# Performance work log

Hardware: AMD Instinct MI355X
Metric: run time of the kernel (lower is better)

The kernel has to match this reference:

```python
import jax, jax.numpy as jnp
import numpy as np

NF, DG, K = 32, 8, 9  # channels, deformable groups, kernel taps (3x3)


def conv2d(x, w, b, stride=1):
    out = jax.lax.conv_general_dilated(x, w, (stride, stride), ((1, 1), (1, 1)),
                                       dimension_numbers=('NCHW', 'OIHW', 'NCHW'))
    return out + b[None, :, None, None]


def lrelu(x):
    return jnp.where(x >= 0, x, 0.1 * x)


def dcn(x, off_fea, om_w, om_b, w, b):
    """Modulated deformable conv v2 (DCN_sep): offsets/mask predicted from off_fea."""
    B, C, H, W = x.shape
    om = conv2d(off_fea, om_w, om_b).reshape(B, DG, 3, K, H, W)
    off_y, off_x = om[:, :, 0], om[:, :, 1]          # [B,DG,K,H,W]
    mask = jax.nn.sigmoid(om[:, :, 2])               # [B,DG,K,H,W]
    ky = (jnp.arange(K) // 3 - 1).astype(x.dtype)    # kernel tap dy in {-1,0,1}
    kx = (jnp.arange(K) % 3 - 1).astype(x.dtype)
    py = off_y + jnp.arange(H, dtype=x.dtype)[:, None] + ky[:, None, None]
    px = off_x + jnp.arange(W, dtype=x.dtype) + kx[:, None, None]
    y0 = jnp.floor(py); x0 = jnp.floor(px)
    dy = py - y0; dx = px - x0
    Cg = C // DG
    xg = x.reshape(B, DG, Cg, H * W)

    def gather(yi, xi):
        valid = ((yi >= 0) & (yi <= H - 1) & (xi >= 0) & (xi <= W - 1)).astype(x.dtype)
        idx = (jnp.clip(yi, 0, H - 1).astype(jnp.int32) * W
               + jnp.clip(xi, 0, W - 1).astype(jnp.int32)).reshape(B, DG, 1, K * H * W)
        v = jnp.take_along_axis(xg, idx, axis=3).reshape(B, DG, Cg, K, H, W)
        return v * valid[:, :, None]  # zero padding outside

    samp = (gather(y0, x0) * ((1 - dy) * (1 - dx))[:, :, None]
            + gather(y0, x0 + 1) * ((1 - dy) * dx)[:, :, None]
            + gather(y0 + 1, x0) * (dy * (1 - dx))[:, :, None]
            + gather(y0 + 1, x0 + 1) * (dy * dx)[:, :, None])
    samp = samp * mask[:, :, None]                   # modulation
    out = jnp.einsum('bgckhw,ogck->bohw', samp, w.reshape(w.shape[0], DG, Cg, K))
    return out + b[None, :, None, None]


def _forward(L1_fea, L1_offset, L2_offset, L3_offset, offset,
             w_l2c1, b_l2c1, w_l2c2, b_l2c2, w_l3c1, b_l3c1, w_l3c2, b_l3c2,
             w_l2fea, b_l2fea, w_l1fea, b_l1fea,
             l3_om_w, l3_om_b, l3_w, l3_b,
             l2_om_w, l2_om_b, l2_w, l2_b,
             l1_om_w, l1_om_b, l1_w, l1_b,
             cas_om_w, cas_om_b, cas_w, cas_b):
    B, C, H, W = L1_fea.shape
    # pyramid feature extraction
    L2 = lrelu(conv2d(L1_fea, w_l2c1, b_l2c1, 2))
    L2 = lrelu(conv2d(L2, w_l2c2, b_l2c2))
    L3 = lrelu(conv2d(L2, w_l3c1, b_l3c1, 2))
    L3 = lrelu(conv2d(L3, w_l3c2, b_l3c2))
    # PCD alignment: coarse-to-fine
    L3f = lrelu(dcn(L3, L3_offset, l3_om_w, l3_om_b, l3_w, l3_b))
    L2f = dcn(L2, L2_offset, l2_om_w, l2_om_b, l2_w, l2_b)
    L3u = jax.image.resize(L3f, (B, C, H // 2, W // 2), 'bilinear')
    L2f = lrelu(conv2d(jnp.concatenate([L2f, L3u], 1), w_l2fea, b_l2fea))
    L1f = dcn(L1_fea, L1_offset, l1_om_w, l1_om_b, l1_w, l1_b)
    L2u = jax.image.resize(L2f, (B, C, H, W), 'bilinear')
    L1f = conv2d(jnp.concatenate([L1f, L2u], 1), w_l1fea, b_l1fea)
    return lrelu(dcn(L1f, offset, cas_om_w, cas_om_b, cas_w, cas_b))


def setup_inputs() -> dict:
    key = jax.random.key(0)
    ks = iter(jax.random.split(key, 64))
    def nrm(shape, s=1.0):
        return jax.random.normal(next(ks), shape, jnp.float32) * s
    B, H, W = 4, 192, 192
    inp = {
        'L1_fea': nrm((B, NF, H, W)),
        'L1_offset': nrm((B, NF, H, W)),
        'L2_offset': nrm((B, NF, H // 2, W // 2)),
        'L3_offset': nrm((B, NF, H // 4, W // 4)),
        'offset': nrm((B, NF, H, W)),
    }
    cs = 1.0 / float(np.sqrt(NF * 9))
    for n, sh in [('w_l2c1', (NF, NF, 3, 3)), ('w_l2c2', (NF, NF, 3, 3)),
                  ('w_l3c1', (NF, NF, 3, 3)), ('w_l3c2', (NF, NF, 3, 3)),
                  ('w_l2fea', (NF, 2 * NF, 3, 3)), ('w_l1fea', (NF, 2 * NF, 3, 3))]:
        inp[n] = nrm(sh, cs)
        inp[n.replace('w_', 'b_')] = jnp.zeros((NF,), jnp.float32)
    for p in ['l3', 'l2', 'l1', 'cas']:
        inp[p + '_om_w'] = nrm((DG * 3 * K, NF, 3, 3), 0.01)  # small => offsets of a few px
        inp[p + '_om_b'] = jnp.zeros((DG * 3 * K,), jnp.float32)
        inp[p + '_w'] = nrm((NF, NF, 3, 3), cs)
        inp[p + '_b'] = jnp.zeros((NF,), jnp.float32)
    return inp


def reference(L1_fea, L1_offset, L2_offset, L3_offset, offset,
              w_l2c1, b_l2c1, w_l2c2, b_l2c2, w_l3c1, b_l3c1, w_l3c2, b_l3c2,
              w_l2fea, b_l2fea, w_l1fea, b_l1fea,
              l3_om_w, l3_om_b, l3_w, l3_b,
              l2_om_w, l2_om_b, l2_w, l2_b,
              l1_om_w, l1_om_b, l1_w, l1_b,
              cas_om_w, cas_om_b, cas_w, cas_b):
    return _forward(L1_fea, L1_offset, L2_offset, L3_offset, offset,
                    w_l2c1, b_l2c1, w_l2c2, b_l2c2, w_l3c1, b_l3c1, w_l3c2, b_l3c2,
                    w_l2fea, b_l2fea, w_l1fea, b_l1fea,
                    l3_om_w, l3_om_b, l3_w, l3_b,
                    l2_om_w, l2_om_b, l2_w, l2_b,
                    l1_om_w, l1_om_b, l1_w, l1_b,
                    cas_om_w, cas_om_b, cas_w, cas_b)
```

## Files before the change

### kernel.cpp

```cpp
#include <hip/hip_runtime.h>
#include <math.h>

#define NFC 32
#define DGC 8

#define CDIV(a, b) (((a) + (b) - 1) / (b))

typedef __attribute__((ext_vector_type(8))) short bf16x8;
typedef __attribute__((ext_vector_type(4))) float f32x4;

__device__ __forceinline__ unsigned short f2bf(float f) {
    unsigned int u = __float_as_uint(f);
    u += 0x7fffu + ((u >> 16) & 1u);
    return (unsigned short)(u >> 16);
}
__device__ __forceinline__ float bf2f(unsigned short s) {
    return __uint_as_float((unsigned int)s << 16);
}
__device__ __forceinline__ float bf_lo(unsigned int u) { return __uint_as_float(u << 16); }
__device__ __forceinline__ float bf_hi(unsigned int u) { return __uint_as_float(u & 0xffff0000u); }

struct Ptr4F { const float* s[4]; };
struct Ptr4U { unsigned short* d[4]; };

__global__ void k_swz_om4(Ptr4F src, Ptr4U dst) {
    const float* w = src.s[blockIdx.y];
    unsigned short* o = dst.d[blockIdx.y];
    int i = blockIdx.x * 256 + threadIdx.x;
    if (i >= 9 * 14 * 64 * 8) return;
    int j  = i & 7;
    int l  = (i >> 3) & 63;
    int nt = (i >> 9) % 14;
    int t  = i / (14 * 512);
    int n  = nt * 16 + (l & 15);
    int ic = (l >> 4) * 8 + j;
    float v = (n < 216) ? w[((size_t)(n * 32 + ic)) * 9 + t] : 0.f;
    o[i] = f2bf(v);
}

template<int ICt>
__global__ void k_swz_wA(Ptr4F src, Ptr4U dst) {
    const int KC = ICt / 32;
    const float* w = src.s[blockIdx.y];
    unsigned short* o = dst.d[blockIdx.y];
    int i = blockIdx.x * 256 + threadIdx.x;
    if (i >= 9 * KC * 1024) return;
    int idx = i;
    int j = idx & 7;   idx >>= 3;
    int l = idx & 63;  idx >>= 6;
    int mt = idx & 1;  idx >>= 1;
    int ck = idx % KC; idx /= KC;
    int t = idx;
    int oc = mt * 16 + (l & 15);
    int ic = ck * 32 + (l >> 4) * 8 + j;
    o[i] = f2bf(w[((size_t)(oc * ICt + ic)) * 9 + t]);
}

__global__ void k_swz_wmA4(Ptr4F src, Ptr4U dst) {
    const float* w = src.s[blockIdx.y];
    unsigned short* o = dst.d[blockIdx.y];
    int i = blockIdx.x * 256 + threadIdx.x;
    if (i >= 9216) return;
    int j  = i & 7;
    int l  = (i >> 3) & 63;
    int mt = (i >> 9) & 1;
    int kc = i >> 10;
    int oc = mt * 16 + (l & 15);
    int k  = kc * 32 + (l >> 4) * 8 + j;
    int ic = k / 9, t = k % 9;
    o[i] = f2bf(w[((size_t)(oc * 32 + ic)) * 9 + t]);
}

__global__ void k_cvt_nhwc(Ptr4F src, Ptr4U dst, int HW, int Btot) {
    const float* in = src.s[blockIdx.y];
    unsigned short* out = dst.d[blockIdx.y];
    int i = blockIdx.x * 256 + threadIdx.x;
    if (i >= Btot * HW * 32) return;
    int c = i & 31;
    int pxf = i >> 5;
    int b = pxf / HW;
    int hw = pxf % HW;
    out[i] = f2bf(in[((size_t)(b * 32 + c)) * HW + hw]);
}

template<int NT, int KC, int STRIDE, bool LRELU>
__global__ __launch_bounds__(256)
void k_conv_mfma(const unsigned short* __restrict__ in1,
                 const unsigned short* __restrict__ in2,
                 const unsigned short* __restrict__ wA,
                 const float* __restrict__ bias,
                 unsigned short* __restrict__ out,
                 int B, int Hin, int Win, int Hout, int Wout) {
    int wid  = (blockIdx.x * 256 + threadIdx.x) >> 6;
    int lane = threadIdx.x & 63;
    int strips = Wout / (16 * NT);
    if (wid >= B * Hout * strips) return;
    int st = wid % strips;
    int h  = (wid / strips) % Hout;
    int b  = wid / (strips * Hout);
    int px0 = st * 16 * NT;

    f32x4 acc[NT][2];
#pragma unroll
    for (int nt = 0; nt < NT; ++nt)
#pragma unroll
        for (int mt = 0; mt < 2; ++mt)
#pragma unroll
            for (int r = 0; r < 4; ++r) acc[nt][mt][r] = 0.f;

    int n  = lane & 15;
    int kq = lane >> 4;

#pragma unroll
    for (int t = 0; t < 9; ++t) {
        int hy = h * STRIDE + t / 3 - 1;
        if (hy < 0 || hy >= Hin) continue;
#pragma unroll
        for (int ck = 0; ck < KC; ++ck) {
            const unsigned short* rowp =
                ((KC == 2 && ck == 1) ? in2 : in1) + ((size_t)(b * Hin + hy) * Win) * 32;
            bf16x8 a0 = *(const bf16x8*)(wA + (size_t)((((t * KC + ck) * 2 + 0) * 64 + lane)) * 8);
            bf16x8 a1 = *(const bf16x8*)(wA + (size_t)((((t * KC + ck) * 2 + 1) * 64 + lane)) * 8);
#pragma unroll
            for (int nt = 0; nt < NT; ++nt) {
                int wx = (px0 + nt * 16 + n) * STRIDE + t % 3 - 1;
                bf16x8 bf;
#pragma unroll
                for (int j = 0; j < 8; ++j) bf[j] = 0;
                if (wx >= 0 && wx < Win)
                    bf = *(const bf16x8*)(rowp + (size_t)wx * 32 + kq * 8);
                acc[nt][0] = __builtin_amdgcn_mfma_f32_16x16x32_bf16(a0, bf, acc[nt][0], 0, 0, 0);
                acc[nt][1] = __builtin_amdgcn_mfma_f32_16x16x32_bf16(a1, bf, acc[nt][1], 0, 0, 0);
            }
        }
    }

    size_t rowbase = ((size_t)(b * Hout + h) * Wout);
#pragma unroll
    for (int mt = 0; mt < 2; ++mt) {
        float4 bs = *(const float4*)(bias + mt * 16 + kq * 4);
#pragma unroll
        for (int nt = 0; nt < NT; ++nt) {
            int px = px0 + nt * 16 + n;
            float v0 = acc[nt][mt][0] + bs.x;
            float v1 = acc[nt][mt][1] + bs.y;
            float v2 = acc[nt][mt][2] + bs.z;
            float v3 = acc[nt][mt][3] + bs.w;
            if (LRELU) {
                v0 = (v0 >= 0.f) ? v0 : 0.1f * v0;
                v1 = (v1 >= 0.f) ? v1 : 0.1f * v1;
                v2 = (v2 >= 0.f) ? v2 : 0.1f * v2;
                v3 = (v3 >= 0.f) ? v3 : 0.1f * v3;
            }
            ushort4 sv = make_ushort4(f2bf(v0), f2bf(v1), f2bf(v2), f2bf(v3));
            *(ushort4*)(out + (rowbase + px) * 32 + mt * 16 + kq * 4) = sv;
        }
    }
}

template<int MODE>
__global__ __launch_bounds__(256)
void k_dcn_fused(const unsigned short* __restrict__ offn,
                 const unsigned short* __restrict__ wswz,
                 const float* __restrict__ om_b,
                 const unsigned short* __restrict__ xn,
                 const unsigned short* __restrict__ wmA,
                 const float* __restrict__ bias,
                 float* __restrict__ outf,
                 unsigned short* __restrict__ outb,
                 int B, int H, int W) {
    const int ROW = 296;
    const int OMR = 36;
    __shared__ __align__(16) unsigned short s_om[216 * OMR];
    __shared__ __align__(16) unsigned short s_samp[32 * ROW];

    int tid = threadIdx.x;
    int lane = tid & 63;
    int wv = tid >> 6;
    int px0 = blockIdx.x * 32;

    {
        int n  = lane & 15;
        int kq = lane >> 4;

        int bmt[2], hmt[2], wmt[2];
#pragma unroll
        for (int mt = 0; mt < 2; ++mt) {
            int p0 = px0 + mt * 16;
            bmt[mt] = p0 / (H * W);
            hmt[mt] = (p0 / W) % H;
            wmt[mt] = p0 % W;
        }

        f32x4 acc[4][2];
#pragma unroll
        for (int i = 0; i < 4; ++i)
#pragma unroll
            for (int mt = 0; mt < 2; ++mt)
#pragma unroll
                for (int r = 0; r < 4; ++r) acc[i][mt][r] = 0.f;

#pragma unroll
        for (int t = 0; t < 9; ++t) {
            bf16x8 a[2];
#pragma unroll
            for (int mt = 0; mt < 2; ++mt) {
#pragma unroll
                for (int j = 0; j < 8; ++j) a[mt][j] = 0;
                int hy = hmt[mt] + t / 3 - 1;
                int wx = wmt[mt] + n + t % 3 - 1;
                if (hy >= 0 && hy < H && wx >= 0 && wx < W)
                    a[mt] = *(const bf16x8*)(offn +
                        (((size_t)(bmt[mt] * H + hy) * W + wx) << 5) + kq * 8);
            }
#pragma unroll
            for (int i = 0; i < 4; ++i) {
                int nt = wv * 4 + i;
                if (nt < 14) {
                    bf16x8 bf = *(const bf16x8*)(wswz + (((size_t)t * 14 + nt) * 64 + lane) * 8);
                    acc[i][0] = __builtin_amdgcn_mfma_f32_16x16x32_bf16(a[0], bf, acc[i][0], 0, 0, 0);
                    acc[i][1] = __builtin_amdgcn_mfma_f32_16x16x32_bf16(a[1], bf, acc[i][1], 0, 0, 0);
                }
            }
        }

#pragma unroll
        for (int i = 0; i < 4; ++i) {
            int nt = wv * 4 + i;
            if (nt < 14) {
                int ch = nt * 16 + n;
                if (ch < 216) {
#pragma unroll
                    for (int mt = 0; mt < 2; ++mt) {
                        ushort4 v = make_ushort4(f2bf(acc[i][mt][0]), f2bf(acc[i][mt][1]),
                                                 f2bf(acc[i][mt][2]), f2bf(acc[i][mt][3]));
                        *(ushort4*)(s_om + ch * OMR + mt * 16 + kq * 4) = v;
                    }
                }
            }
        }
    }
    __syncthreads();

    {
        int px = tid & 31, g = tid >> 5;
        int idx = px0 + px;
        int w = idx % W;
        int h = (idx / W) % H;
        int b = idx / (W * H);

        float om27[27];
#pragma unroll
        for (int j = 0; j < 27; ++j)
            om27[j] = bf2f(s_om[(g * 27 + j) * OMR + px]) + om_b[g * 27 + j];

        const unsigned short* xb = xn + ((size_t)b * H * W) * 32 + g * 4;
        float Hm1 = (float)(H - 1), Wm1 = (float)(W - 1);
        unsigned short arr[36];

#pragma unroll
        for (int k = 0; k < 9; ++k) {
            float mval = 1.f / (1.f + __expf(-om27[18 + k]));
            float py  = om27[k]     + (float)(h + k / 3 - 1);
            float pxx = om27[9 + k] + (float)(w + k % 3 - 1);
            float y0f = floorf(py), x0f = floorf(pxx);
            float dy = py - y0f, dx = pxx - x0f;
            float y1f = y0f + 1.f, x1f = x0f + 1.f;
            float vy0 = (y0f >= 0.f && y0f <= Hm1) ? 1.f : 0.f;
            float vy1 = (y1f >= 0.f && y1f <= Hm1) ? 1.f : 0.f;
            float vx0 = (x0f >= 0.f && x0f <= Wm1) ? 1.f : 0.f;
            float vx1 = (x1f >= 0.f && x1f <= Wm1) ? 1.f : 0.f;
            float w00 = (1.f - dy) * (1.f - dx) * vy0 * vx0;
            float w01 = (1.f - dy) * dx * vy0 * vx1;
            float w10 = dy * (1.f - dx) * vy1 * vx0;
            float w11 = dy * dx * vy1 * vx1;
            int y0c = (int)fminf(fmaxf(y0f, 0.f), Hm1);
            int y1c = (int)fminf(fmaxf(y1f, 0.f), Hm1);
            int x0c = (int)fminf(fmaxf(x0f, 0.f), Wm1);
            int x1c = (int)fminf(fmaxf(x1f, 0.f), Wm1);

            uint2 u00 = *(const uint2*)(xb + ((size_t)y0c * W + x0c) * 32);
            uint2 u01 = *(const uint2*)(xb + ((size_t)y0c * W + x1c) * 32);
            uint2 u10 = *(const uint2*)(xb + ((size_t)y1c * W + x0c) * 32);
            uint2 u11 = *(const uint2*)(xb + ((size_t)y1c * W + x1c) * 32);

            arr[0 * 9 + k] = f2bf((w00 * bf_lo(u00.x) + w01 * bf_lo(u01.x) +
                                   w10 * bf_lo(u10.x) + w11 * bf_lo(u11.x)) * mval);
            arr[1 * 9 + k] = f2bf((w00 * bf_hi(u00.x) + w01 * bf_hi(u01.x) +
                                   w10 * bf_hi(u10.x) + w11 * bf_hi(u11.x)) * mval);
            arr[2 * 9 + k] = f2bf((w00 * bf_lo(u00.y) + w01 * bf_lo(u01.y) +
                                   w10 * bf_lo(u10.y) + w11 * bf_lo(u11.y)) * mval);
            arr[3 * 9 + k] = f2bf((w00 * bf_hi(u00.y) + w01 * bf_hi(u01.y) +
                                   w10 * bf_hi(u10.y) + w11 * bf_hi(u11.y)) * mval);
        }
        ushort4* dst = (ushort4*)(s_samp + px * ROW + g * 36);
        const ushort4* srcp = (const ushort4*)arr;
#pragma unroll
        for (int q = 0; q < 9; ++q) dst[q] = srcp[q];
    }
    __syncthreads();

    int wsid = tid >> 6;
    int mt = wsid & 1, nt2 = wsid >> 1;

    f32x4 acc;
#pragma unroll
    for (int r = 0; r < 4; ++r) acc[r] = 0.f;

    const unsigned short* sb = s_samp + (nt2 * 16 + (lane & 15)) * ROW + (lane >> 4) * 8;
#pragma unroll
    for (int kc = 0; kc < 9; ++kc) {
        bf16x8 a   = *(const bf16x8*)(wmA + ((size_t)(kc * 2 + mt) * 64 + lane) * 8);
        bf16x8 bfr = *(const bf16x8*)(sb + kc * 32);
        acc = __builtin_amdgcn_mfma_f32_16x16x32_bf16(a, bfr, acc, 0, 0, 0);
    }

    int pxg = px0 + nt2 * 16 + (lane & 15);
    int kq = lane >> 4;
    float4 bs = *(const float4*)(bias + mt * 16 + kq * 4);
    float v[4] = {acc[0] + bs.x, acc[1] + bs.y, acc[2] + bs.z, acc[3] + bs.w};
    if (MODE >= 1) {
#pragma unroll
        for (int r = 0; r < 4; ++r) v[r] = (v[r] >= 0.f) ? v[r] : 0.1f * v[r];
    }
    if (MODE == 2) {
        int w2 = pxg % W, h2 = (pxg / W) % H, b2 = pxg / (W * H);
#pragma unroll
        for (int r = 0; r < 4; ++r) {
            int oc = mt * 16 + kq * 4 + r;
            outf[((size_t)(b2 * 32 + oc) * H + h2) * W + w2] = v[r];
        }
    } else {
        ushort4 sv = make_ushort4(f2bf(v[0]), f2bf(v[1]), f2bf(v[2]), f2bf(v[3]));
        *(ushort4*)(outb + (size_t)pxg * 32 + mt * 16 + kq * 4) = sv;
    }
}

__global__ void k_resize2x_nhwc(const unsigned short* __restrict__ in,
                                unsigned short* __restrict__ out,
                                int B, int Hin, int Win) {
    int Hout = Hin * 2, Wout = Win * 2;
    int i = blockIdx.x * 256 + threadIdx.x;
    int total = B * Hout * Wout * 4;
    if (i >= total) return;
    int q  = i & 3;
    int wo = (i >> 2) % Wout;
    int ho = (i >> 2) / Wout % Hout;
    int b  = (i >> 2) / (Wout * Hout);
    float fy = 0.5f * (float)ho - 0.25f;
    float fx = 0.5f * (float)wo - 0.25f;
    float y0f = floorf(fy), x0f = floorf(fx);
    float wy1 = fy - y0f, wx1 = fx - x0f;
    int y0 = max(0, min((int)y0f, Hin - 1));
    int y1 = max(0, min((int)y0f + 1, Hin - 1));
    int x0 = max(0, min((int)x0f, Win - 1));
    int x1 = max(0, min((int)x0f + 1, Win - 1));
    const unsigned short* base = in + ((size_t)b * Hin * Win) * 32 + q * 8;
    const uint4 u00 = *(const uint4*)(base + ((size_t)y0 * Win + x0) * 32);
    const uint4 u01 = *(const uint4*)(base + ((size_t)y0 * Win + x1) * 32);
    const uint4 u10 = *(const uint4*)(base + ((size_t)y1 * Win + x0) * 32);
    const uint4 u11 = *(const uint4*)(base + ((size_t)y1 * Win + x1) * 32);
    float c00 = (1.f - wy1) * (1.f - wx1), c01 = (1.f - wy1) * wx1;
    float c10 = wy1 * (1.f - wx1), c11 = wy1 * wx1;
    const unsigned int* p00 = (const unsigned int*)&u00;
    const unsigned int* p01 = (const unsigned int*)&u01;
    const unsigned int* p10 = (const unsigned int*)&u10;
    const unsigned int* p11 = (const unsigned int*)&u11;
    unsigned int packed[4];
#pragma unroll
    for (int d = 0; d < 4; ++d) {
        float lo = c00 * bf_lo(p00[d]) + c01 * bf_lo(p01[d]) +
                   c10 * bf_lo(p10[d]) + c11 * bf_lo(p11[d]);
        float hi = c00 * bf_hi(p00[d]) + c01 * bf_hi(p01[d]) +
                   c10 * bf_hi(p10[d]) + c11 * bf_hi(p11[d]);
        packed[d] = (unsigned int)f2bf(lo) | ((unsigned int)f2bf(hi) << 16);
    }
    *(uint4*)(out + ((size_t)(b * Hout + ho) * Wout + wo) * 32 + q * 8) =
        make_uint4(packed[0], packed[1], packed[2], packed[3]);
}

extern "C" void kernel_launch(void* const* d_in, const int* in_sizes, int n_in,
                              void* d_out, int out_size, void* d_ws, size_t ws_size,
                              hipStream_t stream) {
    const float* L1_fea = (const float*)d_in[0];
    const float* L1_off = (const float*)d_in[1];
    const float* L2_off = (const float*)d_in[2];
    const float* L3_off = (const float*)d_in[3];
    const float* offset = (const float*)d_in[4];
    const float* w_l2c1 = (const float*)d_in[5];   const float* b_l2c1 = (const float*)d_in[6];
    const float* w_l2c2 = (const float*)d_in[7];   const float* b_l2c2 = (const float*)d_in[8];
    const float* w_l3c1 = (const float*)d_in[9];   const float* b_l3c1 = (const float*)d_in[10];
    const float* w_l3c2 = (const float*)d_in[11];  const float* b_l3c2 = (const float*)d_in[12];
    const float* w_l2fea = (const float*)d_in[13]; const float* b_l2fea = (const float*)d_in[14];
    const float* w_l1fea = (const float*)d_in[15]; const float* b_l1fea = (const float*)d_in[16];
    const float* l3_om_w = (const float*)d_in[17]; const float* l3_om_b = (const float*)d_in[18];
    const float* l3_w = (const float*)d_in[19];    const float* l3_b = (const float*)d_in[20];
    const float* l2_om_w = (const float*)d_in[21]; const float* l2_om_b = (const float*)d_in[22];
    const float* l2_w = (const float*)d_in[23];    const float* l2_b = (const float*)d_in[24];
    const float* l1_om_w = (const float*)d_in[25]; const float* l1_om_b = (const float*)d_in[26];
    const float* l1_w = (const float*)d_in[27];    const float* l1_b = (const float*)d_in[28];
    const float* cas_om_w = (const float*)d_in[29]; const float* cas_om_b = (const float*)d_in[30];
    const float* cas_w = (const float*)d_in[31];   const float* cas_b = (const float*)d_in[32];

    const int B = 4, H1 = 192, W1 = 192, H2 = 96, W2 = 96, H3 = 48, W3 = 48;
    const int HW1 = H1 * W1, HW2 = H2 * W2, HW3 = H3 * W3;

    char* ws = (char*)d_ws;
    size_t cur = 0;
    auto alloc = [&](size_t bytes) {
        char* p = ws + cur;
        cur += (bytes + 255) & ~(size_t)255;
        return p;
    };

    unsigned short* wA_l2c1  = (unsigned short*)alloc(9216 * 2);
    unsigned short* wA_l2c2  = (unsigned short*)alloc(9216 * 2);
    unsigned short* wA_l3c1  = (unsigned short*)alloc(9216 * 2);
    unsigned short* wA_l3c2  = (unsigned short*)alloc(9216 * 2);
    unsigned short* wA_l2fea = (unsigned short*)alloc(18432 * 2);
    unsigned short* wA_l1fea = (unsigned short*)alloc(18432 * 2);
    unsigned short* wmA_l3   = (unsigned short*)alloc(9216 * 2);
    unsigned short* wmA_l2   = (unsigned short*)alloc(9216 * 2);
    unsigned short* wmA_l1   = (unsigned short*)alloc(9216 * 2);
    unsigned short* wmA_cas  = (unsigned short*)alloc(9216 * 2);
    unsigned short* wswz_l3  = (unsigned short*)alloc(64512 * 2);
    unsigned short* wswz_l2  = (unsigned short*)alloc(64512 * 2);
    unsigned short* wswz_l1  = (unsigned short*)alloc(64512 * 2);
    unsigned short* wswz_cas = (unsigned short*)alloc(64512 * 2);

    unsigned short* offn_l3  = (unsigned short*)alloc((size_t)B * 32 * HW3 * 2);
    unsigned short* offn_l2  = (unsigned short*)alloc((size_t)B * 32 * HW2 * 2);
    unsigned short* offn_l1  = (unsigned short*)alloc((size_t)B * 32 * HW1 * 2);
    unsigned short* offn_cas = (unsigned short*)alloc((size_t)B * 32 * HW1 * 2);
    unsigned short* xn_l1    = (unsigned short*)alloc((size_t)B * 32 * HW1 * 2);
    unsigned short* L2a      = (unsigned short*)alloc((size_t)B * 32 * HW2 * 2);
    unsigned short* L2n      = (unsigned short*)alloc((size_t)B * 32 * HW2 * 2);
    unsigned short* L3a      = (unsigned short*)alloc((size_t)B * 32 * HW3 * 2);
    unsigned short* L3n      = (unsigned short*)alloc((size_t)B * 32 * HW3 * 2);
    unsigned short* L3f      = (unsigned short*)alloc((size_t)B * 32 * HW3 * 2);
    unsigned short* L2f_pre  = (unsigned short*)alloc((size_t)B * 32 * HW2 * 2);
    unsigned short* L3u      = (unsigned short*)alloc((size_t)B * 32 * HW2 * 2);
    unsigned short* L2f      = (unsigned short*)alloc((size_t)B * 32 * HW2 * 2);
    unsigned short* L1f_pre  = (unsigned short*)alloc((size_t)B * 32 * HW1 * 2);
    unsigned short* L2u      = (unsigned short*)alloc((size_t)B * 32 * HW1 * 2);
    unsigned short* L1f      = (unsigned short*)alloc((size_t)B * 32 * HW1 * 2);

    {
        Ptr4F s = {{l3_om_w, l2_om_w, l1_om_w, cas_om_w}};
        Ptr4U d = {{wswz_l3, wswz_l2, wswz_l1, wswz_cas}};
        k_swz_om4<<<dim3(CDIV(64512, 256), 4), 256, 0, stream>>>(s, d);
    }
    {
        Ptr4F s = {{w_l2c1, w_l2c2, w_l3c1, w_l3c2}};
        Ptr4U d = {{wA_l2c1, wA_l2c2, wA_l3c1, wA_l3c2}};
        k_swz_wA<32><<<dim3(CDIV(9216, 256), 4), 256, 0, stream>>>(s, d);
    }
    {
        Ptr4F s = {{w_l2fea, w_l1fea, nullptr, nullptr}};
        Ptr4U d = {{wA_l2fea, wA_l1fea, nullptr, nullptr}};
        k_swz_wA<64><<<dim3(CDIV(18432, 256), 2), 256, 0, stream>>>(s, d);
    }
    {
        Ptr4F s = {{l3_w, l2_w, l1_w, cas_w}};
        Ptr4U d = {{wmA_l3, wmA_l2, wmA_l1, wmA_cas}};
        k_swz_wmA4<<<dim3(CDIV(9216, 256), 4), 256, 0, stream>>>(s, d);
    }

    {
        Ptr4F s = {{L1_off, offset, L1_fea, nullptr}};
        Ptr4U d = {{offn_l1, offn_cas, xn_l1, nullptr}};
        k_cvt_nhwc<<<dim3(CDIV(B * 32 * HW1, 256), 3), 256, 0, stream>>>(s, d, HW1, B);
    }
    {
        Ptr4F s = {{L2_off, nullptr, nullptr, nullptr}};
        Ptr4U d = {{offn_l2, nullptr, nullptr, nullptr}};
        k_cvt_nhwc<<<dim3(CDIV(B * 32 * HW2, 256), 1), 256, 0, stream>>>(s, d, HW2, B);
    }
    {
        Ptr4F s = {{L3_off, nullptr, nullptr, nullptr}};
        Ptr4U d = {{offn_l3, nullptr, nullptr, nullptr}};
        k_cvt_nhwc<<<dim3(CDIV(B * 32 * HW3, 256), 1), 256, 0, stream>>>(s, d, HW3, B);
    }

    k_conv_mfma<3, 1, 2, true><<<CDIV(B * H2 * 2, 4), 256, 0, stream>>>(
        xn_l1, nullptr, wA_l2c1, b_l2c1, L2a, B, H1, W1, H2, W2);
    k_conv_mfma<3, 1, 1, true><<<CDIV(B * H2 * 2, 4), 256, 0, stream>>>(
        L2a, nullptr, wA_l2c2, b_l2c2, L2n, B, H2, W2, H2, W2);
    k_conv_mfma<3, 1, 2, true><<<CDIV(B * H3 * 1, 4), 256, 0, stream>>>(
        L2n, nullptr, wA_l3c1, b_l3c1, L3a, B, H2, W2, H3, W3);
    k_conv_mfma<3, 1, 1, true><<<CDIV(B * H3 * 1, 4), 256, 0, stream>>>(
        L3a, nullptr, wA_l3c2, b_l3c2, L3n, B, H3, W3, H3, W3);

    k_dcn_fused<1><<<B * HW3 / 32, 256, 0, stream>>>(
        offn_l3, wswz_l3, l3_om_b, L3n, wmA_l3, l3_b, nullptr, L3f, B, H3, W3);

    k_dcn_fused<0><<<B * HW2 / 32, 256, 0, stream>>>(
        offn_l2, wswz_l2, l2_om_b, L2n, wmA_l2, l2_b, nullptr, L2f_pre, B, H2, W2);
    k_resize2x_nhwc<<<CDIV(B * HW2 * 4, 256), 256, 0, stream>>>(L3f, L3u, B, H3, W3);
    k_conv_mfma<3, 2, 1, true><<<CDIV(B * H2 * 2, 4), 256, 0, stream>>>(
        L2f_pre, L3u, wA_l2fea, b_l2fea, L2f, B, H2, W2, H2, W2);

    k_dcn_fused<0><<<B * HW1 / 32, 256, 0, stream>>>(
        offn_l1, wswz_l1, l1_om_b, xn_l1, wmA_l1, l1_b, nullptr, L1f_pre, B, H1, W1);
    k_resize2x_nhwc<<<CDIV(B * HW1 * 4, 256), 256, 0, stream>>>(L2f, L2u, B, H2, W2);
    k_conv_mfma<4, 2, 1, false><<<CDIV(B * H1 * 3, 4), 256, 0, stream>>>(
        L1f_pre, L2u, wA_l1fea, b_l1fea, L1f, B, H1, W1, H1, W1);

    k_dcn_fused<2><<<B * HW1 / 32, 256, 0, stream>>>(
        offn_cas, wswz_cas, cas_om_b, L1f, wmA_cas, cas_b, (float*)d_out, nullptr, B, H1, W1);
}
```

Before: 606.8 us.

## Use group-major feature layout for DCN bilinear gathers

Adds a group-planar copy of each DCN input feature map ([B,8,H,W,4] bf16), produced either by a new conversion kernel or as an extra store in the preceding conv epilogue. The DCN sampler reads from this copy, so the x-neighbour pair for a tap sits in adjacent 8-byte words and clamping uses integer math with select-based edge handling. This aims to make the scattered gathers more cache-friendly and cheaper to address. The cost is extra writes and one extra conversion pass. The s_om padding also changes from 36 to 32, which may affect LDS bank conflicts.

```diff
diff --git a/kernel.cpp b/kernel.cpp
--- a/kernel.cpp
+++ b/kernel.cpp
@@ -83,13 +83,26 @@
     out[i] = f2bf(in[((size_t)(b * 32 + c)) * HW + hw]);
 }
 
-template<int NT, int KC, int STRIDE, bool LRELU>
+__global__ void k_cvt_xg(const unsigned short* __restrict__ in,
+                         unsigned short* __restrict__ out, int HW, int B) {
+    int i = blockIdx.x * 256 + threadIdx.x;
+    if (i >= B * HW * 8) return;
+    int g = i & 7;
+    int pxf = i >> 3;
+    int b = pxf / HW;
+    int hw = pxf % HW;
+    uint2 v = *(const uint2*)(in + (size_t)pxf * 32 + g * 4);
+    *(uint2*)(out + (((size_t)(b * 8 + g) * HW) + hw) * 4) = v;
+}
+
+template<int NT, int KC, int STRIDE, bool LRELU, bool XG>
 __global__ __launch_bounds__(256)
 void k_conv_mfma(const unsigned short* __restrict__ in1,
                  const unsigned short* __restrict__ in2,
                  const unsigned short* __restrict__ wA,
                  const float* __restrict__ bias,
                  unsigned short* __restrict__ out,
+                 unsigned short* __restrict__ outg,
                  int B, int Hin, int Win, int Hout, int Wout) {
     int wid  = (blockIdx.x * 256 + threadIdx.x) >> 6;
     int lane = threadIdx.x & 63;
@@ -154,6 +167,10 @@
             }
             ushort4 sv = make_ushort4(f2bf(v0), f2bf(v1), f2bf(v2), f2bf(v3));
             *(ushort4*)(out + (rowbase + px) * 32 + mt * 16 + kq * 4) = sv;
+            if (XG) {
+                int g = mt * 4 + kq;
+                *(ushort4*)(outg + (((size_t)(b * 8 + g) * Hout + h) * Wout + px) * 4) = sv;
+            }
         }
     }
 }
@@ -163,14 +180,14 @@
 void k_dcn_fused(const unsigned short* __restrict__ offn,
                  const unsigned short* __restrict__ wswz,
                  const float* __restrict__ om_b,
-                 const unsigned short* __restrict__ xn,
+                 const unsigned short* __restrict__ xg,
                  const unsigned short* __restrict__ wmA,
                  const float* __restrict__ bias,
                  float* __restrict__ outf,
                  unsigned short* __restrict__ outb,
                  int B, int H, int W) {
     const int ROW = 296;
-    const int OMR = 36;
+    const int OMR = 32;
     __shared__ __align__(16) unsigned short s_om[216 * OMR];
     __shared__ __align__(16) unsigned short s_samp[32 * ROW];
 
@@ -254,8 +271,8 @@
         for (int j = 0; j < 27; ++j)
             om27[j] = bf2f(s_om[(g * 27 + j) * OMR + px]) + om_b[g * 27 + j];
 
-        const unsigned short* xb = xn + ((size_t)b * H * W) * 32 + g * 4;
-        float Hm1 = (float)(H - 1), Wm1 = (float)(W - 1);
+        const unsigned short* xb = xg + ((size_t)(b * 8 + g) * H * W) * 4;
+        float Hm1 = (float)(H - 1);
         unsigned short arr[36];
 
 #pragma unroll
@@ -265,33 +282,49 @@
             float pxx = om27[9 + k] + (float)(w + k % 3 - 1);
             float y0f = floorf(py), x0f = floorf(pxx);
             float dy = py - y0f, dx = pxx - x0f;
-            float y1f = y0f + 1.f, x1f = x0f + 1.f;
+            int iy0 = (int)y0f, ix0 = (int)x0f;
+
             float vy0 = (y0f >= 0.f && y0f <= Hm1) ? 1.f : 0.f;
-            float vy1 = (y1f >= 0.f && y1f <= Hm1) ? 1.f : 0.f;
-            float vx0 = (x0f >= 0.f && x0f <= Wm1) ? 1.f : 0.f;
-            float vx1 = (x1f >= 0.f && x1f <= Wm1) ? 1.f : 0.f;
-            float w00 = (1.f - dy) * (1.f - dx) * vy0 * vx0;
-            float w01 = (1.f - dy) * dx * vy0 * vx1;
-            float w10 = dy * (1.f - dx) * vy1 * vx0;
-            float w11 = dy * dx * vy1 * vx1;
-            int y0c = (int)fminf(fmaxf(y0f, 0.f), Hm1);
-            int y1c = (int)fminf(fmaxf(y1f, 0.f), Hm1);
-            int x0c = (int)fminf(fmaxf(x0f, 0.f), Wm1);
-            int x1c = (int)fminf(fmaxf(x1f, 0.f), Wm1);
-
-            uint2 u00 = *(const uint2*)(xb + ((size_t)y0c * W + x0c) * 32);
-            uint2 u01 = *(const uint2*)(xb + ((size_t)y0c * W + x1c) * 32);
-            uint2 u10 = *(const uint2*)(xb + ((size_t)y1c * W + x0c) * 32);
-            uint2 u11 = *(const uint2*)(xb + ((size_t)y1c * W + x1c) * 32);
-
-            arr[0 * 9 + k] = f2bf((w00 * bf_lo(u00.x) + w01 * bf_lo(u01.x) +
-                                   w10 * bf_lo(u10.x) + w11 * bf_lo(u11.x)) * mval);
-            arr[1 * 9 + k] = f2bf((w00 * bf_hi(u00.x) + w01 * bf_hi(u01.x) +
-                                   w10 * bf_hi(u10.x) + w11 * bf_hi(u11.x)) * mval);
-            arr[2 * 9 + k] = f2bf((w00 * bf_lo(u00.y) + w01 * bf_lo(u01.y) +
-                                   w10 * bf_lo(u10.y) + w11 * bf_lo(u11.y)) * mval);
-            arr[3 * 9 + k] = f2bf((w00 * bf_hi(u00.y) + w01 * bf_hi(u01.y) +
-                                   w10 * bf_hi(u10.y) + w11 * bf_hi(u11.y)) * mval);
+            float vy1 = (y0f + 1.f >= 0.f && y0f + 1.f <= Hm1) ? 1.f : 0.f;
+            float vx0 = (ix0 >= 0 && ix0 <= W - 1) ? 1.f : 0.f;
+            float vx1 = (ix0 + 1 >= 0 && ix0 + 1 <= W - 1) ? 1.f : 0.f;
+            float wx0 = (1.f - dx) * vx0;
+            float wx1 = dx * vx1;
+            float wy0 = (1.f - dy) * vy0 * mval;
+            float wy1 = dy * vy1 * mval;
+
+            int y0c = min(max(iy0, 0), H - 1);
+            int y1c = min(max(iy0 + 1, 0), H - 1);
+            int bx  = min(max(ix0, 0), W - 2);
+
+            const unsigned short* r0p = xb + ((size_t)y0c * W + bx) * 4;
+            const unsigned short* r1p = xb + ((size_t)y1c * W + bx) * 4;
+            uint2 a0 = *(const uint2*)r0p;
+            uint2 b0 = *(const uint2*)(r0p + 4);
+            uint2 a1 = *(const uint2*)r1p;
+            uint2 b1 = *(const uint2*)(r1p + 4);
+
+            bool hi0 = (ix0 >= W - 1);
+            bool lo1 = (ix0 < 0);
+            uint2 sx0r0 = hi0 ? b0 : a0;
+            uint2 sx1r0 = lo1 ? a0 : b0;
+            uint2 sx0r1 = hi0 ? b1 : a1;
+            uint2 sx1r1 = lo1 ? a1 : b1;
+
+#pragma unroll
+            for (int c = 0; c < 4; ++c) {
+                float v00 = (c & 1) ? bf_hi(((const unsigned int*)&sx0r0)[c >> 1])
+                                    : bf_lo(((const unsigned int*)&sx0r0)[c >> 1]);
+                float v01 = (c & 1) ? bf_hi(((const unsigned int*)&sx1r0)[c >> 1])
+                                    : bf_lo(((const unsigned int*)&sx1r0)[c >> 1]);
+                float v10 = (c & 1) ? bf_hi(((const unsigned int*)&sx0r1)[c >> 1])
+                                    : bf_lo(((const unsigned int*)&sx0r1)[c >> 1]);
+                float v11 = (c & 1) ? bf_hi(((const unsigned int*)&sx1r1)[c >> 1])
+                                    : bf_lo(((const unsigned int*)&sx1r1)[c >> 1]);
+                float r0 = wx0 * v00 + wx1 * v01;
+                float r1 = wx0 * v10 + wx1 * v11;
+                arr[c * 9 + k] = f2bf(wy0 * r0 + wy1 * r1);
+            }
         }
         ushort4* dst = (ushort4*)(s_samp + px * ROW + g * 36);
         const ushort4* srcp = (const ushort4*)arr;
@@ -433,10 +466,13 @@
     unsigned short* offn_l1  = (unsigned short*)alloc((size_t)B * 32 * HW1 * 2);
     unsigned short* offn_cas = (unsigned short*)alloc((size_t)B * 32 * HW1 * 2);
     unsigned short* xn_l1    = (unsigned short*)alloc((size_t)B * 32 * HW1 * 2);
+    unsigned short* L1g      = (unsigned short*)alloc((size_t)B * 32 * HW1 * 2);
     unsigned short* L2a      = (unsigned short*)alloc((size_t)B * 32 * HW2 * 2);
     unsigned short* L2n      = (unsigned short*)alloc((size_t)B * 32 * HW2 * 2);
+    unsigned short* L2g      = (unsigned short*)alloc((size_t)B * 32 * HW2 * 2);
     unsigned short* L3a      = (unsigned short*)alloc((size_t)B * 32 * HW3 * 2);
     unsigned short* L3n      = (unsigned short*)alloc((size_t)B * 32 * HW3 * 2);
+    unsigned short* L3g      = (unsigned short*)alloc((size_t)B * 32 * HW3 * 2);
     unsigned short* L3f      = (unsigned short*)alloc((size_t)B * 32 * HW3 * 2);
     unsigned short* L2f_pre  = (unsigned short*)alloc((size_t)B * 32 * HW2 * 2);
     unsigned short* L3u      = (unsigned short*)alloc((size_t)B * 32 * HW2 * 2);
@@ -444,6 +480,7 @@
     unsigned short* L1f_pre  = (unsigned short*)alloc((size_t)B * 32 * HW1 * 2);
     unsigned short* L2u      = (unsigned short*)alloc((size_t)B * 32 * HW1 * 2);
     unsigned short* L1f      = (unsigned short*)alloc((size_t)B * 32 * HW1 * 2);
+    unsigned short* L1fg     = (unsigned short*)alloc((size_t)B * 32 * HW1 * 2);
 
     {
         Ptr4F s = {{l3_om_w, l2_om_w, l1_om_w, cas_om_w}};
@@ -481,31 +518,32 @@
         Ptr4U d = {{offn_l3, nullptr, nullptr, nullptr}};
         k_cvt_nhwc<<<dim3(CDIV(B * 32 * HW3, 256), 1), 256, 0, stream>>>(s, d, HW3, B);
     }
-
-    k_conv_mfma<3, 1, 2, true><<<CDIV(B * H2 * 2, 4), 256, 0, stream>>>(
-        xn_l1, nullptr, wA_l2c1, b_l2c1, L2a, B, H1, W1, H2, W2);
-    k_conv_mfma<3, 1, 1, true><<<CDIV(B * H2 * 2, 4), 256, 0, stream>>>(
-        L2a, nullptr, wA_l2c2, b_l2c2, L2n, B, H2, W2, H2, W2);
-    k_conv_mfma<3, 1, 2, true><<<CDIV(B * H3 * 1, 4), 256, 0, stream>>>(
-        L2n, nullptr, wA_l3c1, b_l3c1, L3a, B, H2, W2, H3, W3);
-    k_conv_mfma<3, 1, 1, true><<<CDIV(B * H3 * 1, 4), 256, 0, stream>>>(
-        L3a, nullptr, wA_l3c2, b_l3c2, L3n, B, H3, W3, H3, W3);
+    k_cvt_xg<<<CDIV(B * HW1 * 8, 256), 256, 0, stream>>>(xn_l1, L1g, HW1, B);
+
+    k_conv_mfma<3, 1, 2, true, false><<<CDIV(B * H2 * 2, 4), 256, 0, stream>>>(
+        xn_l1, nullptr, wA_l2c1, b_l2c1, L2a, nullptr, B, H1, W1, H2, W2);
+    k_conv_mfma<3, 1, 1, true, true><<<CDIV(B * H2 * 2, 4), 256, 0, stream>>>(
+        L2a, nullptr, wA_l2c2, b_l2c2, L2n, L2g, B, H2, W2, H2, W2);
+    k_conv_mfma<3, 1, 2, true, false><<<CDIV(B * H3 * 1, 4), 256, 0, stream>>>(
+        L2n, nullptr, wA_l3c1, b_l3c1, L3a, nullptr, B, H2, W2, H3, W3);
+    k_conv_mfma<3, 1, 1, true, true><<<CDIV(B * H3 * 1, 4), 256, 0, stream>>>(
+        L3a, nullptr, wA_l3c2, b_l3c2, L3n, L3g, B, H3, W3, H3, W3);
 
     k_dcn_fused<1><<<B * HW3 / 32, 256, 0, stream>>>(
-        offn_l3, wswz_l3, l3_om_b, L3n, wmA_l3, l3_b, nullptr, L3f, B, H3, W3);
+        offn_l3, wswz_l3, l3_om_b, L3g, wmA_l3, l3_b, nullptr, L3f, B, H3, W3);
 
     k_dcn_fused<0><<<B * HW2 / 32, 256, 0, stream>>>(
-        offn_l2, wswz_l2, l2_om_b, L2n, wmA_l2, l2_b, nullptr, L2f_pre, B, H2, W2);
+        offn_l2, wswz_l2, l2_om_b, L2g, wmA_l2, l2_b, nullptr, L2f_pre, B, H2, W2);
     k_resize2x_nhwc<<<CDIV(B * HW2 * 4, 256), 256, 0, stream>>>(L3f, L3u, B, H3, W3);
-    k_conv_mfma<3, 2, 1, true><<<CDIV(B * H2 * 2, 4), 256, 0, stream>>>(
-        L2f_pre, L3u, wA_l2fea, b_l2fea, L2f, B, H2, W2, H2, W2);
+    k_conv_mfma<3, 2, 1, true, false><<<CDIV(B * H2 * 2, 4), 256, 0, stream>>>(
+        L2f_pre, L3u, wA_l2fea, b_l2fea, L2f, nullptr, B, H2, W2, H2, W2);
 
     k_dcn_fused<0><<<B * HW1 / 32, 256, 0, stream>>>(
-        offn_l1, wswz_l1, l1_om_b, xn_l1, wmA_l1, l1_b, nullptr, L1f_pre, B, H1, W1);
+        offn_l1, wswz_l1, l1_om_b, L1g, wmA_l1, l1_b, nullptr, L1f_pre, B, H1, W1);
     k_resize2x_nhwc<<<CDIV(B * HW1 * 4, 256), 256, 0, stream>>>(L2f, L2u, B, H2, W2);
-    k_conv_mfma<4, 2, 1, false><<<CDIV(B * H1 * 3, 4), 256, 0, stream>>>(
-        L1f_pre, L2u, wA_l1fea, b_l1fea, L1f, B, H1, W1, H1, W1);
+    k_conv_mfma<4, 2, 1, false, true><<<CDIV(B * H1 * 3, 4), 256, 0, stream>>>(
+        L1f_pre, L2u, wA_l1fea, b_l1fea, L1f, L1fg, B, H1, W1, H1, W1);
 
     k_dcn_fused<2><<<B * HW1 / 32, 256, 0, stream>>>(
-        offn_cas, wswz_cas, cas_om_b, L1f, wmA_cas, cas_b, (float*)d_out, nullptr, B, H1, W1);
-}
+        offn_cas, wswz_cas, cas_om_b, L1fg, wmA_cas, cas_b, (float*)d_out, nullptr, B, H1, W1);
+}
```

After: 627.0 us. 3.3% more time.
